# Performance work log

Measured on AMD Instinct MI355X. Metric: run time of the kernel, lower is better.

The kernel has to match this reference:

```python
import jax, jax.numpy as jnp
import numpy as np

B, F, A, U = 4096, 64, 8, 32  # batch, n_features, num_att, n_outputs
R = 2.0                       # the 'r' scaling inside exp(kernel * r)


def setup_inputs() -> dict:
    key = jax.random.key(0)
    k1, k2 = jax.random.split(key)
    inputs = jax.random.normal(k1, (B, F), dtype=jnp.float32)
    # per-exclusion-feature attention kernels, stacked: [F, A, F, U]
    limit = float(np.sqrt(6.0 / (F + U)))  # glorot_uniform
    kernels = jax.random.uniform(k2, (F, A, F, U), dtype=jnp.float32,
                                 minval=-limit, maxval=limit)
    return {"inputs": inputs, "kernels": kernels}


def reference(inputs, kernels):
    # inputs: [B, F]; kernels: [j=F excluded-feature index, A, F, U]
    f = inputs.shape[-1]
    mask = 1.0 - jnp.eye(f, dtype=inputs.dtype)          # [j, F]: zero out feature j
    xm = mask[:, None, :] * inputs[None, :, :]           # [j, B, F]
    z = jnp.einsum('jbf,jafu->jabu', xm, kernels)        # [j, A, B, U]
    z = jax.nn.softmax(z, axis=-1)                       # softmax over units
    w = jnp.exp(kernels * R)                             # [j, A, F, U]
    scores = jnp.einsum('jabu,jafu->jabf', z, w)         # [j, A, B, F]
    scores = scores.mean(axis=0)                         # mean over exclusion axis -> [A, B, F]
    return jax.nn.softmax(scores, axis=-1)               # [A, B, F]
```

## Files before the change

kernel.cpp:

```cpp
#include <hip/hip_runtime.h>
#include <hip/hip_bf16.h>
#include <math.h>

#define B_ 4096
#define F_ 64
#define A_ 8
#define U_ 32

typedef float f32x4 __attribute__((ext_vector_type(4)));
typedef short bf16x8 __attribute__((ext_vector_type(8)));

#define KD_OFF (4ull << 20)

static __device__ __forceinline__ unsigned int pk_bf16(float lo, float hi) {
    union { __hip_bfloat162 h2; unsigned int u; } cv;
    cv.h2 = __float22bfloat162_rn(make_float2(lo, hi));
    return cv.u;
}
static __device__ __forceinline__ float rb(float f) {
    unsigned int u = __float_as_uint(f);
    u += 0x7FFFu + ((u >> 16) & 1u);
    return __uint_as_float(u & 0xFFFF0000u);
}

__global__ __launch_bounds__(256) void ife_prep(const float* __restrict__ kern,
                                                unsigned char* __restrict__ ws)
{
    const int bid = blockIdx.x;
    const int a = bid >> 6, j = bid & 63;
    const int t = threadIdx.x;
    __shared__ float st[64][36];

    const float* src = kern + ((size_t)j * A_ + a) * (F_ * U_);
    {
        const int f = t >> 2, u0 = (t & 3) * 8;
        *(float4*)&st[f][u0]     = *(const float4*)&src[f * U_ + u0];
        *(float4*)&st[f][u0 + 4] = *(const float4*)&src[f * U_ + u0 + 4];
    }
    __syncthreads();

    unsigned char* dst = ws + (size_t)bid * 8192;
    const int fragid = t >> 6, lane = t & 63, q = lane >> 4, c = lane & 15;

    {
        const int kc = fragid >> 1, ut = fragid & 1;
        const int f0 = kc * 32 + q * 8, u = ut * 16 + c;
        unsigned int w[4];
        #pragma unroll
        for (int i = 0; i < 4; ++i)
            w[i] = pk_bf16(st[f0 + 2 * i][u], st[f0 + 2 * i + 1][u]);
        *(uint4*)(dst + fragid * 1024 + lane * 16) = make_uint4(w[0], w[1], w[2], w[3]);
    }
    {
        const int f = fragid * 16 + c;
        const float4 wa = *(const float4*)&st[f][q * 4];
        const float4 wb = *(const float4*)&st[f][16 + q * 4];
        unsigned int w[4];
        w[0] = pk_bf16(__expf(2.f * wa.x), __expf(2.f * wa.y));
        w[1] = pk_bf16(__expf(2.f * wa.z), __expf(2.f * wa.w));
        w[2] = pk_bf16(__expf(2.f * wb.x), __expf(2.f * wb.y));
        w[3] = pk_bf16(__expf(2.f * wb.z), __expf(2.f * wb.w));
        *(uint4*)(dst + 4096 + fragid * 1024 + lane * 16) = make_uint4(w[0], w[1], w[2], w[3]);
    }
    if (t < U_)
        ((float*)(ws + KD_OFF))[(size_t)bid * U_ + t] = rb(st[j][t]);
}

__global__ __launch_bounds__(512, 4) void ife_main(const float* __restrict__ x,
                                                   const unsigned char* __restrict__ ws,
                                                   float* __restrict__ out)
{
    const int a = blockIdx.y, bt = blockIdx.x, t = threadIdx.x;
    const int wv = t >> 6, lane = t & 63, q = lane >> 4, c = lane & 15;
    const int grp = wv >> 2, w4 = wv & 3;

    __shared__ __align__(16) float SH[6272];
    __shared__ __align__(16) unsigned char Fbuf[2][2][8192];
    float* Xf = SH;
    float* Kd = SH + 4224;

    bf16x8 Xh[2];
    {
        const float* xr = x + (size_t)(bt * 64 + w4 * 16 + c) * F_;
        #pragma unroll
        for (int kc = 0; kc < 2; ++kc) {
            const float4 va = *(const float4*)&xr[kc * 32 + q * 8];
            const float4 vb = *(const float4*)&xr[kc * 32 + q * 8 + 4];
            union { unsigned int u[4]; bf16x8 v; } H;
            H.u[0] = pk_bf16(va.x, va.y);
            H.u[1] = pk_bf16(va.z, va.w);
            H.u[2] = pk_bf16(vb.x, vb.y);
            H.u[3] = pk_bf16(vb.z, vb.w);
            Xh[kc] = H.v;
        }
    }
    {
        const int row = t >> 3, cb = (t & 7) * 8;
        const float* xsrc = x + (size_t)(bt * 64 + row) * F_ + cb;
        const float4 v0 = *(const float4*)&xsrc[0];
        const float4 v1 = *(const float4*)&xsrc[4];
        float* xd = Xf + row * 66 + cb;
        xd[0] = rb(v0.x); xd[1] = rb(v0.y); xd[2] = rb(v0.z); xd[3] = rb(v0.w);
        xd[4] = rb(v1.x); xd[5] = rb(v1.y); xd[6] = rb(v1.z); xd[7] = rb(v1.w);
    }
    {
        const float* kd = (const float*)(ws + KD_OFF) + (size_t)a * 64 * U_;
        const int jj = t >> 3, u0 = (t & 7) * 4;
        *(float4*)&Kd[jj * 32 + u0] = *(const float4*)&kd[jj * U_ + u0];
    }

    const unsigned char* blob = ws + (size_t)a * 64 * 8192;
    const f32x4 vzero = (f32x4){0.f, 0.f, 0.f, 0.f};

    union { unsigned int u[4]; bf16x8 v; } oc;
    oc.u[0] = 0x3F803F80u; oc.u[1] = 0x3F803F80u; oc.u[2] = 0x3F803F80u; oc.u[3] = 0x3F803F80u;
    const bf16x8 ONES = oc.v;

    f32x4 S0 = vzero, S1 = vzero, S2 = vzero, S3 = vzero;

    typedef const __attribute__((address_space(1))) unsigned int gau32;
    typedef __attribute__((address_space(3))) unsigned int lau32;
    auto STAGE = [&](int buf, int s) {
        const int tg = wv >> 2, fp = wv & 3;
        const int jt = tg * 32 + s;
        const unsigned char* g = blob + (size_t)jt * 8192 + fp * 2048 + lane * 16;
        unsigned char* l = &Fbuf[buf][tg][fp * 2048];
        __builtin_amdgcn_global_load_lds((gau32*)(g),        (lau32*)(l),        16, 0, 0);
        __builtin_amdgcn_global_load_lds((gau32*)(g + 1024), (lau32*)(l + 1024), 16, 0, 0);
    };

    const int jb = grp * 32;
    const int xfrow = (w4 * 16 + c) * 66;

    STAGE(0, 0);
    __syncthreads();

    int cur = 0;
    #pragma unroll 1
    for (int s = 0; s < 32; ++s) {
        if (s < 31) STAGE(cur ^ 1, s + 1);

        const unsigned char* pt = &Fbuf[cur][grp][lane * 16];
        const int j = jb + s;

        const bf16x8 K0 = *(const bf16x8*)(pt);
        const bf16x8 K1 = *(const bf16x8*)(pt + 1024);
        const bf16x8 K2 = *(const bf16x8*)(pt + 2048);
        const bf16x8 K3 = *(const bf16x8*)(pt + 3072);

        const float xj = Xf[xfrow + j];
        const f32x4 kda = *(const f32x4*)&Kd[j * 32 + q * 4];
        const f32x4 kdb = *(const f32x4*)&Kd[j * 32 + 16 + q * 4];

        f32x4 ZA = vzero, ZB = vzero;
        ZA = __builtin_amdgcn_mfma_f32_16x16x32_bf16(K0, Xh[0], ZA, 0, 0, 0);
        ZA = __builtin_amdgcn_mfma_f32_16x16x32_bf16(K2, Xh[1], ZA, 0, 0, 0);
        ZB = __builtin_amdgcn_mfma_f32_16x16x32_bf16(K1, Xh[0], ZB, 0, 0, 0);
        ZB = __builtin_amdgcn_mfma_f32_16x16x32_bf16(K3, Xh[1], ZB, 0, 0, 0);

        const bf16x8 W0 = *(const bf16x8*)(pt + 4096);
        const bf16x8 W1 = *(const bf16x8*)(pt + 5120);
        const bf16x8 W2 = *(const bf16x8*)(pt + 6144);
        const bf16x8 W3 = *(const bf16x8*)(pt + 7168);

        union { unsigned int u[4]; bf16x8 v; } E;
        E.u[0] = pk_bf16(__expf(ZA[0] - xj * kda[0]), __expf(ZA[1] - xj * kda[1]));
        E.u[1] = pk_bf16(__expf(ZA[2] - xj * kda[2]), __expf(ZA[3] - xj * kda[3]));
        E.u[2] = pk_bf16(__expf(ZB[0] - xj * kdb[0]), __expf(ZB[1] - xj * kdb[1]));
        E.u[3] = pk_bf16(__expf(ZB[2] - xj * kdb[2]), __expf(ZB[3] - xj * kdb[3]));

        const f32x4 sv = __builtin_amdgcn_mfma_f32_16x16x32_bf16(ONES, E.v, vzero, 0, 0, 0);

        const f32x4 D0 = __builtin_amdgcn_mfma_f32_16x16x32_bf16(W0, E.v, vzero, 0, 0, 0);
        const f32x4 D1 = __builtin_amdgcn_mfma_f32_16x16x32_bf16(W1, E.v, vzero, 0, 0, 0);
        const f32x4 D2 = __builtin_amdgcn_mfma_f32_16x16x32_bf16(W2, E.v, vzero, 0, 0, 0);
        const f32x4 D3 = __builtin_amdgcn_mfma_f32_16x16x32_bf16(W3, E.v, vzero, 0, 0, 0);

        const float inv = __builtin_amdgcn_rcpf(sv[0]);
        #pragma unroll
        for (int r = 0; r < 4; ++r) {
            S0[r] += D0[r] * inv;
            S1[r] += D1[r] * inv;
            S2[r] += D2[r] * inv;
            S3[r] += D3[r] * inv;
        }

        __syncthreads();
        cur ^= 1;
    }

    float* Sred = SH;
    if (grp == 1) {
        float* pp = Sred + (size_t)(w4 * 64 + lane) * 20;
        *(f32x4*)(pp + 0)  = S0;
        *(f32x4*)(pp + 4)  = S1;
        *(f32x4*)(pp + 8)  = S2;
        *(f32x4*)(pp + 12) = S3;
    }
    __syncthreads();
    if (grp == 0) {
        const float* pp = Sred + (size_t)(w4 * 64 + lane) * 20;
        S0 += *(const f32x4*)(pp + 0);
        S1 += *(const f32x4*)(pp + 4);
        S2 += *(const f32x4*)(pp + 8);
        S3 += *(const f32x4*)(pp + 12);

        const float sc = 1.f / 64.f;
        float ex[4][4];
        float part = 0.f;
        #pragma unroll
        for (int r = 0; r < 4; ++r) {
            ex[0][r] = __expf(S0[r] * sc);
            ex[1][r] = __expf(S1[r] * sc);
            ex[2][r] = __expf(S2[r] * sc);
            ex[3][r] = __expf(S3[r] * sc);
            part += ex[0][r] + ex[1][r] + ex[2][r] + ex[3][r];
        }
        part += __shfl_xor(part, 16, 64);
        part += __shfl_xor(part, 32, 64);
        const float inv = 1.f / part;

        const int b = bt * 64 + w4 * 16 + c;
        float* o = out + ((size_t)a * B_ + b) * F_;
        #pragma unroll
        for (int ft = 0; ft < 4; ++ft) {
            float4 v;
            v.x = ex[ft][0] * inv;
            v.y = ex[ft][1] * inv;
            v.z = ex[ft][2] * inv;
            v.w = ex[ft][3] * inv;
            *(float4*)&o[ft * 16 + q * 4] = v;
        }
    }
}

extern "C" void kernel_launch(void* const* d_in, const int* in_sizes, int n_in,
                              void* d_out, int out_size, void* d_ws, size_t ws_size,
                              hipStream_t stream) {
    (void)in_sizes; (void)n_in; (void)out_size; (void)ws_size;
    const float* x    = (const float*)d_in[0];
    const float* kern = (const float*)d_in[1];
    float* out        = (float*)d_out;
    unsigned char* ws = (unsigned char*)d_ws;

    hipLaunchKernelGGL(ife_prep, dim3(F_ * A_), dim3(256), 0, stream, kern, ws);
    hipLaunchKernelGGL(ife_main, dim3(B_ / 64, A_), dim3(512), 0, stream, x, ws, out);
}
```

Baseline: 96.16 us.

## Split exclusion axis four ways and reuse each K/W fragment over two row blocks

Each wave now handles 32 batch rows (two 16-row MFMA blocks) rather than 16. The eight waves split the 64 exclusion indices into four groups of 16, and the main loop shrinks from 32 to 16 iterations. Every K/W fragment read from LDS therefore feeds twice as many MFMAs, and the number of per-iteration block barriers is halved. The x and kd tables are kept in LDS as bf16 to make room for the larger 4-tile double buffer. The cost is more live registers, a larger shared-memory footprint that could reduce occupancy, and a final cross-group reduction through LDS that now sums four partials.

```diff
diff --git a/kernel.cpp b/kernel.cpp
--- a/kernel.cpp
+++ b/kernel.cpp
@@ -21,6 +21,14 @@
     unsigned int u = __float_as_uint(f);
     u += 0x7FFFu + ((u >> 16) & 1u);
     return __uint_as_float(u & 0xFFFF0000u);
+}
+static __device__ __forceinline__ unsigned short fbits(float f) {
+    unsigned int u = __float_as_uint(f);
+    u += 0x7FFFu + ((u >> 16) & 1u);
+    return (unsigned short)(u >> 16);
+}
+static __device__ __forceinline__ float b2f(unsigned short h) {
+    return __uint_as_float((unsigned int)h << 16);
 }
 
 __global__ __launch_bounds__(256) void ife_prep(const float* __restrict__ kern,
@@ -72,16 +80,16 @@
 {
     const int a = blockIdx.y, bt = blockIdx.x, t = threadIdx.x;
     const int wv = t >> 6, lane = t & 63, q = lane >> 4, c = lane & 15;
-    const int grp = wv >> 2, w4 = wv & 3;
-
-    __shared__ __align__(16) float SH[6272];
-    __shared__ __align__(16) unsigned char Fbuf[2][2][8192];
-    float* Xf = SH;
-    float* Kd = SH + 4224;
-
-    bf16x8 Xh[2];
-    {
-        const float* xr = x + (size_t)(bt * 64 + w4 * 16 + c) * F_;
+    const int jg = wv >> 1, rh = wv & 1;
+
+    __shared__ __align__(16) unsigned short Xf_h[64 * 66];
+    __shared__ __align__(16) unsigned short Kd_h[64 * 32];
+    __shared__ __align__(16) unsigned char Fbuf[2][4][8192];
+
+    bf16x8 Xh[2][2];
+    #pragma unroll
+    for (int rb_ = 0; rb_ < 2; ++rb_) {
+        const float* xr = x + (size_t)(bt * 64 + rh * 32 + rb_ * 16 + c) * F_;
         #pragma unroll
         for (int kc = 0; kc < 2; ++kc) {
             const float4 va = *(const float4*)&xr[kc * 32 + q * 8];
@@ -91,7 +99,7 @@
             H.u[1] = pk_bf16(va.z, va.w);
             H.u[2] = pk_bf16(vb.x, vb.y);
             H.u[3] = pk_bf16(vb.z, vb.w);
-            Xh[kc] = H.v;
+            Xh[rb_][kc] = H.v;
         }
     }
     {
@@ -99,14 +107,20 @@
         const float* xsrc = x + (size_t)(bt * 64 + row) * F_ + cb;
         const float4 v0 = *(const float4*)&xsrc[0];
         const float4 v1 = *(const float4*)&xsrc[4];
-        float* xd = Xf + row * 66 + cb;
-        xd[0] = rb(v0.x); xd[1] = rb(v0.y); xd[2] = rb(v0.z); xd[3] = rb(v0.w);
-        xd[4] = rb(v1.x); xd[5] = rb(v1.y); xd[6] = rb(v1.z); xd[7] = rb(v1.w);
+        unsigned short* xd = &Xf_h[row * 66 + cb];
+        xd[0] = fbits(v0.x); xd[1] = fbits(v0.y); xd[2] = fbits(v0.z); xd[3] = fbits(v0.w);
+        xd[4] = fbits(v1.x); xd[5] = fbits(v1.y); xd[6] = fbits(v1.z); xd[7] = fbits(v1.w);
     }
     {
         const float* kd = (const float*)(ws + KD_OFF) + (size_t)a * 64 * U_;
         const int jj = t >> 3, u0 = (t & 7) * 4;
-        *(float4*)&Kd[jj * 32 + u0] = *(const float4*)&kd[jj * U_ + u0];
+        const float4 v = *(const float4*)&kd[jj * U_ + u0];
+        ushort4 us;
+        us.x = (unsigned short)(__float_as_uint(v.x) >> 16);
+        us.y = (unsigned short)(__float_as_uint(v.y) >> 16);
+        us.z = (unsigned short)(__float_as_uint(v.z) >> 16);
+        us.w = (unsigned short)(__float_as_uint(v.w) >> 16);
+        *(ushort4*)&Kd_h[jj * 32 + u0] = us;
     }
 
     const unsigned char* blob = ws + (size_t)a * 64 * 8192;
@@ -116,120 +130,163 @@
     oc.u[0] = 0x3F803F80u; oc.u[1] = 0x3F803F80u; oc.u[2] = 0x3F803F80u; oc.u[3] = 0x3F803F80u;
     const bf16x8 ONES = oc.v;
 
-    f32x4 S0 = vzero, S1 = vzero, S2 = vzero, S3 = vzero;
+    f32x4 S[2][4];
+    #pragma unroll
+    for (int rb_ = 0; rb_ < 2; ++rb_) {
+        S[rb_][0] = vzero; S[rb_][1] = vzero; S[rb_][2] = vzero; S[rb_][3] = vzero;
+    }
 
     typedef const __attribute__((address_space(1))) unsigned int gau32;
     typedef __attribute__((address_space(3))) unsigned int lau32;
     auto STAGE = [&](int buf, int s) {
-        const int tg = wv >> 2, fp = wv & 3;
-        const int jt = tg * 32 + s;
-        const unsigned char* g = blob + (size_t)jt * 8192 + fp * 2048 + lane * 16;
-        unsigned char* l = &Fbuf[buf][tg][fp * 2048];
+        const int tile = wv >> 1, half = wv & 1;
+        const int jt = tile * 16 + s;
+        const unsigned char* g = blob + (size_t)jt * 8192 + half * 4096 + lane * 16;
+        unsigned char* l = &Fbuf[buf][tile][half * 4096];
         __builtin_amdgcn_global_load_lds((gau32*)(g),        (lau32*)(l),        16, 0, 0);
         __builtin_amdgcn_global_load_lds((gau32*)(g + 1024), (lau32*)(l + 1024), 16, 0, 0);
+        __builtin_amdgcn_global_load_lds((gau32*)(g + 2048), (lau32*)(l + 2048), 16, 0, 0);
+        __builtin_amdgcn_global_load_lds((gau32*)(g + 3072), (lau32*)(l + 3072), 16, 0, 0);
     };
-
-    const int jb = grp * 32;
-    const int xfrow = (w4 * 16 + c) * 66;
 
     STAGE(0, 0);
     __syncthreads();
 
     int cur = 0;
     #pragma unroll 1
-    for (int s = 0; s < 32; ++s) {
-        if (s < 31) STAGE(cur ^ 1, s + 1);
-
-        const unsigned char* pt = &Fbuf[cur][grp][lane * 16];
-        const int j = jb + s;
+    for (int s = 0; s < 16; ++s) {
+        if (s < 15) STAGE(cur ^ 1, s + 1);
+
+        const unsigned char* pt = &Fbuf[cur][jg][lane * 16];
+        const int j = jg * 16 + s;
 
         const bf16x8 K0 = *(const bf16x8*)(pt);
         const bf16x8 K1 = *(const bf16x8*)(pt + 1024);
         const bf16x8 K2 = *(const bf16x8*)(pt + 2048);
         const bf16x8 K3 = *(const bf16x8*)(pt + 3072);
 
-        const float xj = Xf[xfrow + j];
-        const f32x4 kda = *(const f32x4*)&Kd[j * 32 + q * 4];
-        const f32x4 kdb = *(const f32x4*)&Kd[j * 32 + 16 + q * 4];
-
-        f32x4 ZA = vzero, ZB = vzero;
-        ZA = __builtin_amdgcn_mfma_f32_16x16x32_bf16(K0, Xh[0], ZA, 0, 0, 0);
-        ZA = __builtin_amdgcn_mfma_f32_16x16x32_bf16(K2, Xh[1], ZA, 0, 0, 0);
-        ZB = __builtin_amdgcn_mfma_f32_16x16x32_bf16(K1, Xh[0], ZB, 0, 0, 0);
-        ZB = __builtin_amdgcn_mfma_f32_16x16x32_bf16(K3, Xh[1], ZB, 0, 0, 0);
+        const ushort4 ka = *(const ushort4*)&Kd_h[j * 32 + q * 4];
+        const ushort4 kb = *(const ushort4*)&Kd_h[j * 32 + 16 + q * 4];
+        const float xj0 = b2f(Xf_h[(rh * 32 + c) * 66 + j]);
+        const float xj1 = b2f(Xf_h[(rh * 32 + 16 + c) * 66 + j]);
+        f32x4 kda, kdb;
+        kda[0] = b2f(ka.x); kda[1] = b2f(ka.y); kda[2] = b2f(ka.z); kda[3] = b2f(ka.w);
+        kdb[0] = b2f(kb.x); kdb[1] = b2f(kb.y); kdb[2] = b2f(kb.z); kdb[3] = b2f(kb.w);
+
+        f32x4 ZA0 = vzero, ZB0 = vzero, ZA1 = vzero, ZB1 = vzero;
+        ZA0 = __builtin_amdgcn_mfma_f32_16x16x32_bf16(K0, Xh[0][0], ZA0, 0, 0, 0);
+        ZA0 = __builtin_amdgcn_mfma_f32_16x16x32_bf16(K2, Xh[0][1], ZA0, 0, 0, 0);
+        ZB0 = __builtin_amdgcn_mfma_f32_16x16x32_bf16(K1, Xh[0][0], ZB0, 0, 0, 0);
+        ZB0 = __builtin_amdgcn_mfma_f32_16x16x32_bf16(K3, Xh[0][1], ZB0, 0, 0, 0);
+        ZA1 = __builtin_amdgcn_mfma_f32_16x16x32_bf16(K0, Xh[1][0], ZA1, 0, 0, 0);
+        ZA1 = __builtin_amdgcn_mfma_f32_16x16x32_bf16(K2, Xh[1][1], ZA1, 0, 0, 0);
+        ZB1 = __builtin_amdgcn_mfma_f32_16x16x32_bf16(K1, Xh[1][0], ZB1, 0, 0, 0);
+        ZB1 = __builtin_amdgcn_mfma_f32_16x16x32_bf16(K3, Xh[1][1], ZB1, 0, 0, 0);
 
         const bf16x8 W0 = *(const bf16x8*)(pt + 4096);
         const bf16x8 W1 = *(const bf16x8*)(pt + 5120);
         const bf16x8 W2 = *(const bf16x8*)(pt + 6144);
         const bf16x8 W3 = *(const bf16x8*)(pt + 7168);
 
-        union { unsigned int u[4]; bf16x8 v; } E;
-        E.u[0] = pk_bf16(__expf(ZA[0] - xj * kda[0]), __expf(ZA[1] - xj * kda[1]));
-        E.u[1] = pk_bf16(__expf(ZA[2] - xj * kda[2]), __expf(ZA[3] - xj * kda[3]));
-        E.u[2] = pk_bf16(__expf(ZB[0] - xj * kdb[0]), __expf(ZB[1] - xj * kdb[1]));
-        E.u[3] = pk_bf16(__expf(ZB[2] - xj * kdb[2]), __expf(ZB[3] - xj * kdb[3]));
-
-        const f32x4 sv = __builtin_amdgcn_mfma_f32_16x16x32_bf16(ONES, E.v, vzero, 0, 0, 0);
-
-        const f32x4 D0 = __builtin_amdgcn_mfma_f32_16x16x32_bf16(W0, E.v, vzero, 0, 0, 0);
-        const f32x4 D1 = __builtin_amdgcn_mfma_f32_16x16x32_bf16(W1, E.v, vzero, 0, 0, 0);
-        const f32x4 D2 = __builtin_amdgcn_mfma_f32_16x16x32_bf16(W2, E.v, vzero, 0, 0, 0);
-        const f32x4 D3 = __builtin_amdgcn_mfma_f32_16x16x32_bf16(W3, E.v, vzero, 0, 0, 0);
-
-        const float inv = __builtin_amdgcn_rcpf(sv[0]);
-        #pragma unroll
-        for (int r = 0; r < 4; ++r) {
-            S0[r] += D0[r] * inv;
-            S1[r] += D1[r] * inv;
-            S2[r] += D2[r] * inv;
-            S3[r] += D3[r] * inv;
+        {
+            union { unsigned int u[4]; bf16x8 v; } E;
+            E.u[0] = pk_bf16(__expf(ZA0[0] - xj0 * kda[0]), __expf(ZA0[1] - xj0 * kda[1]));
+            E.u[1] = pk_bf16(__expf(ZA0[2] - xj0 * kda[2]), __expf(ZA0[3] - xj0 * kda[3]));
+            E.u[2] = pk_bf16(__expf(ZB0[0] - xj0 * kdb[0]), __expf(ZB0[1] - xj0 * kdb[1]));
+            E.u[3] = pk_bf16(__expf(ZB0[2] - xj0 * kdb[2]), __expf(ZB0[3] - xj0 * kdb[3]));
+            const f32x4 sv = __builtin_amdgcn_mfma_f32_16x16x32_bf16(ONES, E.v, vzero, 0, 0, 0);
+            const f32x4 D0 = __builtin_amdgcn_mfma_f32_16x16x32_bf16(W0, E.v, vzero, 0, 0, 0);
+            const f32x4 D1 = __builtin_amdgcn_mfma_f32_16x16x32_bf16(W1, E.v, vzero, 0, 0, 0);
+            const f32x4 D2 = __builtin_amdgcn_mfma_f32_16x16x32_bf16(W2, E.v, vzero, 0, 0, 0);
+            const f32x4 D3 = __builtin_amdgcn_mfma_f32_16x16x32_bf16(W3, E.v, vzero, 0, 0, 0);
+            const float inv = __builtin_amdgcn_rcpf(sv[0]);
+            #pragma unroll
+            for (int r = 0; r < 4; ++r) {
+                S[0][0][r] += D0[r] * inv;
+                S[0][1][r] += D1[r] * inv;
+                S[0][2][r] += D2[r] * inv;
+                S[0][3][r] += D3[r] * inv;
+            }
+        }
+        {
+            union { unsigned int u[4]; bf16x8 v; } E;
+            E.u[0] = pk_bf16(__expf(ZA1[0] - xj1 * kda[0]), __expf(ZA1[1] - xj1 * kda[1]));
+            E.u[1] = pk_bf16(__expf(ZA1[2] - xj1 * kda[2]), __expf(ZA1[3] - xj1 * kda[3]));
+            E.u[2] = pk_bf16(__expf(ZB1[0] - xj1 * kdb[0]), __expf(ZB1[1] - xj1 * kdb[1]));
+            E.u[3] = pk_bf16(__expf(ZB1[2] - xj1 * kdb[2]), __expf(ZB1[3] - xj1 * kdb[3]));
+            const f32x4 sv = __builtin_amdgcn_mfma_f32_16x16x32_bf16(ONES, E.v, vzero, 0, 0, 0);
+            const f32x4 D0 = __builtin_amdgcn_mfma_f32_16x16x32_bf16(W0, E.v, vzero, 0, 0, 0);
+            const f32x4 D1 = __builtin_amdgcn_mfma_f32_16x16x32_bf16(W1, E.v, vzero, 0, 0, 0);
+            const f32x4 D2 = __builtin_amdgcn_mfma_f32_16x16x32_bf16(W2, E.v, vzero, 0, 0, 0);
+            const f32x4 D3 = __builtin_amdgcn_mfma_f32_16x16x32_bf16(W3, E.v, vzero, 0, 0, 0);
+            const float inv = __builtin_amdgcn_rcpf(sv[0]);
+            #pragma unroll
+            for (int r = 0; r < 4; ++r) {
+                S[1][0][r] += D0[r] * inv;
+                S[1][1][r] += D1[r] * inv;
+                S[1][2][r] += D2[r] * inv;
+                S[1][3][r] += D3[r] * inv;
+            }
         }
 
         __syncthreads();
         cur ^= 1;
     }
 
-    float* Sred = SH;
-    if (grp == 1) {
-        float* pp = Sred + (size_t)(w4 * 64 + lane) * 20;
-        *(f32x4*)(pp + 0)  = S0;
-        *(f32x4*)(pp + 4)  = S1;
-        *(f32x4*)(pp + 8)  = S2;
-        *(f32x4*)(pp + 12) = S3;
+    float* Sred = (float*)Fbuf;
+    {
+        float* pp = Sred + ((size_t)wv * 64 + lane) * 32;
+        #pragma unroll
+        for (int rb_ = 0; rb_ < 2; ++rb_)
+            #pragma unroll
+            for (int ft = 0; ft < 4; ++ft)
+                *(f32x4*)(pp + rb_ * 16 + ft * 4) = S[rb_][ft];
     }
     __syncthreads();
-    if (grp == 0) {
-        const float* pp = Sred + (size_t)(w4 * 64 + lane) * 20;
-        S0 += *(const f32x4*)(pp + 0);
-        S1 += *(const f32x4*)(pp + 4);
-        S2 += *(const f32x4*)(pp + 8);
-        S3 += *(const f32x4*)(pp + 12);
+    if (jg == 0) {
+        f32x4 F[2][4];
+        #pragma unroll
+        for (int rb_ = 0; rb_ < 2; ++rb_) {
+            F[rb_][0] = vzero; F[rb_][1] = vzero; F[rb_][2] = vzero; F[rb_][3] = vzero;
+        }
+        #pragma unroll
+        for (int g = 0; g < 4; ++g) {
+            const float* pp = Sred + ((size_t)(g * 2 + rh) * 64 + lane) * 32;
+            #pragma unroll
+            for (int rb_ = 0; rb_ < 2; ++rb_)
+                #pragma unroll
+                for (int ft = 0; ft < 4; ++ft)
+                    F[rb_][ft] += *(const f32x4*)(pp + rb_ * 16 + ft * 4);
+        }
 
         const float sc = 1.f / 64.f;
-        float ex[4][4];
-        float part = 0.f;
-        #pragma unroll
-        for (int r = 0; r < 4; ++r) {
-            ex[0][r] = __expf(S0[r] * sc);
-            ex[1][r] = __expf(S1[r] * sc);
-            ex[2][r] = __expf(S2[r] * sc);
-            ex[3][r] = __expf(S3[r] * sc);
-            part += ex[0][r] + ex[1][r] + ex[2][r] + ex[3][r];
-        }
-        part += __shfl_xor(part, 16, 64);
-        part += __shfl_xor(part, 32, 64);
-        const float inv = 1.f / part;
-
-        const int b = bt * 64 + w4 * 16 + c;
-        float* o = out + ((size_t)a * B_ + b) * F_;
-        #pragma unroll
-        for (int ft = 0; ft < 4; ++ft) {
-            float4 v;
-            v.x = ex[ft][0] * inv;
-            v.y = ex[ft][1] * inv;
-            v.z = ex[ft][2] * inv;
-            v.w = ex[ft][3] * inv;
-            *(float4*)&o[ft * 16 + q * 4] = v;
+        #pragma unroll
+        for (int rb_ = 0; rb_ < 2; ++rb_) {
+            float ex[4][4];
+            float part = 0.f;
+            #pragma unroll
+            for (int r = 0; r < 4; ++r) {
+                ex[0][r] = __expf(F[rb_][0][r] * sc);
+                ex[1][r] = __expf(F[rb_][1][r] * sc);
+                ex[2][r] = __expf(F[rb_][2][r] * sc);
+                ex[3][r] = __expf(F[rb_][3][r] * sc);
+                part += ex[0][r] + ex[1][r] + ex[2][r] + ex[3][r];
+            }
+            part += __shfl_xor(part, 16, 64);
+            part += __shfl_xor(part, 32, 64);
+            const float inv = 1.f / part;
+
+            const int b = bt * 64 + rh * 32 + rb_ * 16 + c;
+            float* o = out + ((size_t)a * B_ + b) * F_;
+            #pragma unroll
+            for (int ft = 0; ft < 4; ++ft) {
+                float4 v;
+                v.x = ex[ft][0] * inv;
+                v.y = ex[ft][1] * inv;
+                v.z = ex[ft][2] * inv;
+                v.w = ex[ft][3] * inv;
+                *(float4*)&o[ft * 16 + q * 4] = v;
+            }
         }
     }
 }
```

After: 101.2 us. 1.05x slower.
